# Optimization experiments

Hardware: AMD Instinct MI355X
Metric: run time of the kernel (lower is better)

The kernel has to match this reference:

```python
import jax, jax.numpy as jnp
import numpy as np

NUM_EMBEDDINGS = 1024
EMBEDDING_DIM = 256
COMMITMENT_COST = 0.25


def setup_inputs() -> dict:
    key = jax.random.key(0)
    k_z, k_e = jax.random.split(key)
    z = jax.random.normal(k_z, (4, EMBEDDING_DIM, 16, 32, 32), dtype=jnp.float32)
    # torch init: uniform_(-1/K, 1/K)
    emb = jax.random.uniform(
        k_e, (NUM_EMBEDDINGS, EMBEDDING_DIM), dtype=jnp.float32,
        minval=-1.0 / NUM_EMBEDDINGS, maxval=1.0 / NUM_EMBEDDINGS)
    return {"z": z, "emb": emb}


def reference(z, emb):
    sg = jax.lax.stop_gradient
    b, c, d, h, w = z.shape
    K = emb.shape[0]
    # (B,C,D,H,W) -> (N, C)
    z_flat = jnp.transpose(z, (0, 2, 3, 4, 1)).reshape(-1, c)
    x_sq = jnp.sum(z_flat * z_flat, axis=1, keepdims=True)          # (N,1)
    e_sq = jnp.sum(emb * emb, axis=1)                                # (K,)
    xe = z_flat @ emb.T                                              # (N,K)
    distances = x_sq + e_sq[None, :] - 2.0 * xe
    encoding_indices = jnp.argmin(distances, axis=1)                 # (N,)
    z_q = emb[encoding_indices].reshape(b, d, h, w, c).transpose(0, 4, 1, 2, 3)
    embedding_loss = jnp.mean((sg(z_q) - z) ** 2)
    commitment_loss = COMMITMENT_COST * jnp.mean((z_q - sg(z)) ** 2)
    vq_loss = embedding_loss + commitment_loss
    z_q_st = z + sg(z_q - z)  # straight-through
    # perplexity from codebook usage histogram (== mean of one-hot encodings)
    counts = jnp.zeros((K,), z_flat.dtype).at[encoding_indices].add(1.0)
    avg_probs = counts / z_flat.shape[0]
    perplexity = jnp.exp(-jnp.sum(avg_probs * jnp.log(avg_probs + 1e-10)))
    return z_q_st, vq_loss, perplexity, encoding_indices.reshape(b, d, h, w)
```

## Files before the change

kernel.cpp:

```cpp
#include <hip/hip_runtime.h>


#define C_DIM 256
#define K_CODES 1024
#define N_VEC 65536
#define T_GAP 4e-4f

#define OUT_ZQ_SIZE 16777216
#define OUT_LOSS_OFF 16777216
#define OUT_PP_OFF   16777217
#define OUT_IDX_OFF  16777218

#define WS_EH    0
#define WS_EL    524288
#define WS_ESQ   1048576
#define WS_XSQ   1052672
#define WS_CNT   1314816
#define WS_LOSS  1318912
#define WS_FLC   1318920
#define WS_FLIST 1581072
#define WS_PM1   1843264
#define WS_EMBT  1843264
#define WS_PM2   2891840
#define WS_PIX   3940416

typedef __attribute__((ext_vector_type(8))) short short8;
typedef __attribute__((ext_vector_type(8))) unsigned short ushort8;
typedef __attribute__((ext_vector_type(16))) float f32x16;

__device__ __forceinline__ unsigned short bf16_rne(float v) {
    unsigned u = __float_as_uint(v);
    unsigned r = (u + 0x7FFFu + ((u >> 16) & 1u)) >> 16;
    return (unsigned short)r;
}



__global__ __launch_bounds__(256) void convert_z_kernel(const float* __restrict__ z,
                                                        unsigned short* __restrict__ zhF,
                                                        unsigned short* __restrict__ zlF,
                                                        float* __restrict__ xsq) {
#pragma clang fp contract(off)
    __shared__ float tile[128][65];
    const int tid = threadIdx.x;
    const int ln = tid & 63;
    const int og = tid >> 6;
    const int n0 = blockIdx.x * 64;
    const int b = n0 >> 14, s0 = n0 & 16383;
    const int n = n0 + ln;
    const size_t tbase = (size_t)(n >> 5) * 8192;
    const int lr = n & 31;
    float res = 0.0f;

    for (int p = 0; p < 2; ++p) {
        __syncthreads();
        for (int i = 0; i < 32; ++i) {
            int c = p * 128 + i * 4 + og;
            tile[i * 4 + og][ln] = z[((size_t)b << 22) + ((size_t)c << 14) + s0 + ln];
        }
        __syncthreads();
#pragma unroll
        for (int t = 0; t < 4; ++t) {
            int oh = og + t * 4;
            int o  = p * 16 + oh;
            ushort8 hb, lb;
#pragma unroll
            for (int j = 0; j < 8; ++j) {
                float v = tile[oh * 8 + j][ln];
                unsigned short h = bf16_rne(v);
                hb[j] = h;
                lb[j] = bf16_rne(v - __uint_as_float((unsigned)h << 16));
            }
            size_t off = tbase + (size_t)(o >> 1) * 512 + (size_t)(lr + 32 * (o & 1)) * 8;
            *reinterpret_cast<ushort8*>(zhF + off) = hb;
            *reinterpret_cast<ushort8*>(zlF + off) = lb;
        }
        if (tid < 64) {
            float r[8];
#pragma unroll
            for (int j = 0; j < 8; ++j) { float v = tile[j][tid]; r[j] = v * v; }
#pragma unroll
            for (int i = 8; i < 128; i += 8)
#pragma unroll
                for (int j = 0; j < 8; ++j) { float v = tile[i + j][tid]; float t2 = v * v; r[j] = r[j] + t2; }
            float blk = ((r[0] + r[1]) + (r[2] + r[3])) + ((r[4] + r[5]) + (r[6] + r[7]));
            res = (p == 0) ? blk : res + blk;
        }
    }
    if (tid < 64) xsq[n0 + tid] = res;
}

__device__ __forceinline__ float pairwise_sq_128(const float* p) {
#pragma clang fp contract(off)
    float r[8];
#pragma unroll
    for (int j = 0; j < 8; ++j) { float v = p[j]; r[j] = v * v; }
#pragma unroll
    for (int i = 8; i < 128; i += 8)
#pragma unroll
        for (int j = 0; j < 8; ++j) { float v = p[i + j]; float t = v * v; r[j] = r[j] + t; }
    return ((r[0] + r[1]) + (r[2] + r[3])) + ((r[4] + r[5]) + (r[6] + r[7]));
}

__global__ __launch_bounds__(256) void convert_e_kernel(const float* __restrict__ emb,
                                                        unsigned short* __restrict__ ehF,
                                                        unsigned short* __restrict__ elF,
                                                        float* __restrict__ esq) {
#pragma clang fp contract(off)
    int t = blockIdx.x * 256 + threadIdx.x;
    int k = t >> 5, o = t & 31;
    int c0 = o * 8;
    ushort8 hb, lb;
#pragma unroll
    for (int j = 0; j < 8; ++j) {
        float v = emb[k * C_DIM + c0 + j];
        unsigned short h = bf16_rne(v);
        hb[j] = h;
        lb[j] = bf16_rne(v - __uint_as_float((unsigned)h << 16));
    }
    size_t off = (size_t)(k >> 5) * 8192 + (size_t)(o >> 1) * 512 + (size_t)((k & 31) + 32 * (o & 1)) * 8;
    *reinterpret_cast<ushort8*>(ehF + off) = hb;
    *reinterpret_cast<ushort8*>(elF + off) = lb;
    if (threadIdx.x < 8) {
        int k8 = blockIdx.x * 8 + threadIdx.x;
        const float* row = emb + (size_t)k8 * C_DIM;
        esq[k8] = pairwise_sq_128(row) + pairwise_sq_128(row + 128);
    }
}

__global__ __launch_bounds__(256) void transpose_kernel(const float* __restrict__ emb,
                                                        float* __restrict__ embT) {
    __shared__ float t[64][65];
    const int k0 = blockIdx.x * 64;
    const int c0 = blockIdx.y * 64;
    const int tx = threadIdx.x & 63, ty = threadIdx.x >> 6;
    for (int r = ty; r < 64; r += 4)
        t[r][tx] = emb[(k0 + r) * C_DIM + c0 + tx];
    __syncthreads();
    for (int r = ty; r < 64; r += 4)
        embT[(c0 + r) * K_CODES + k0 + tx] = t[tx][r];
}


__global__ __launch_bounds__(512, 1) void screen_kernel(
    const unsigned short* __restrict__ zhF, const unsigned short* __restrict__ zlF,
    const unsigned short* __restrict__ ehF, const unsigned short* __restrict__ elF,
    const float* __restrict__ esq, const float* __restrict__ xsq,
    float* __restrict__ pm1, float* __restrict__ pm2,
    unsigned short* __restrict__ pix) {
    __shared__ __align__(16) unsigned short abuf[2][64 * 512];
    __shared__ float xbuf[512];
    __shared__ float smp1[2][8][64], smp2[2][8][64];
    __shared__ int   smi[2][8][64];

    const int tid = threadIdx.x;
    const int w = tid >> 6, l = tid & 63, lr = l & 31, lh = l >> 5;
    const int bid = blockIdx.x;
    const int v = (bid & 7) * 64 + (bid >> 3);
    const int nb = v >> 2, kb = v & 3;
    const int n0 = nb * 512;
    const int kw = kb * 256 + w * 32;
    const int loff = l * 8;

    short8 Eh[16], El[16];
    {
        const unsigned short* bh = ehF + (size_t)(kb * 8 + w) * 8192 + loff;
        const unsigned short* bl = elF + (size_t)(kb * 8 + w) * 8192 + loff;
#pragma unroll
        for (int q = 0; q < 16; ++q) {
            Eh[q] = *reinterpret_cast<const short8*>(bh + q * 512);
            Bl_dummy:;
            El[q] = *reinterpret_cast<const short8*>(bl + q * 512);
        }
    }
    float esql[16];
#pragma unroll
    for (int r = 0; r < 16; ++r)
        esql[r] = esq[kw + (r & 3) + 8 * (r >> 2) + 4 * lh];

    __builtin_amdgcn_global_load_lds(
        (const __attribute__((address_space(1))) void*)(xsq + n0 + w * 64 + l),
        (__attribute__((address_space(3))) void*)&xbuf[w * 64], 4, 0, 0);

    asm volatile("s_waitcnt vmcnt(0)" ::: "memory");
    __builtin_amdgcn_s_barrier();

#define STAGE(S) do {                                                                   \
    const int _b = (S) & 1;                                                             \
    _Pragma("unroll")                                                                   \
    for (int ci = 0; ci < 8; ++ci) {                                                    \
        int c = 8 * w + ci;                                                             \
        const unsigned short* src = ((c & 32) ? zlF : zhF)                              \
            + (size_t)((n0 >> 5) + (S) * 2 + ((c >> 4) & 1)) * 8192                     \
            + (size_t)(c & 15) * 512 + loff;                                            \
        __builtin_amdgcn_global_load_lds(                                               \
            (const __attribute__((address_space(1))) void*)src,                         \
            (__attribute__((address_space(3))) void*)&abuf[_b][c * 512], 16, 0, 0);     \
    }                                                                                   \
} while (0)

    STAGE(0);

    float rm1 = 3.4e38f, rm2 = 3.4e38f;
    int   ri1 = 0;

    for (int s = 0; s < 8; ++s) {
        const int cur = s & 1;
        asm volatile("s_waitcnt vmcnt(0) lgkmcnt(0)" ::: "memory");
        __builtin_amdgcn_s_barrier();
        __builtin_amdgcn_sched_barrier(0);
        if (s < 7) STAGE(s + 1);

        if (s >= 1 && w == s - 1) {
            const int pp = (s - 1) & 1;
            float m1 = smp1[pp][0][l], m2 = smp2[pp][0][l];
            int i1 = smi[pp][0][l];
#pragma unroll
            for (int ww = 1; ww < 8; ++ww) {
                float q1 = smp1[pp][ww][l], q2 = smp2[pp][ww][l];
                int qi = smi[pp][ww][l];
                if (q1 < m1)      { m2 = fminf(m1, q2); m1 = q1; i1 = qi; }
                else if (q1 > m1) { m2 = fminf(m2, q1); }
                else              { m2 = m1; }
            }
            rm1 = m1; rm2 = m2; ri1 = i1;
        }

        f32x16 acc0, acc1;
#pragma unroll
        for (int r = 0; r < 16; ++r) { acc0[r] = 0.0f; acc1[r] = 0.0f; }

        __builtin_amdgcn_s_setprio(1);
#pragma unroll
        for (int q = 0; q < 16; ++q) {
            short8 azh0 = *reinterpret_cast<const short8*>(&abuf[cur][(q)      * 512 + loff]);
            short8 azh1 = *reinterpret_cast<const short8*>(&abuf[cur][(16 + q) * 512 + loff]);
            short8 azl0 = *reinterpret_cast<const short8*>(&abuf[cur][(32 + q) * 512 + loff]);
            short8 azl1 = *reinterpret_cast<const short8*>(&abuf[cur][(48 + q) * 512 + loff]);
            acc0 = __builtin_amdgcn_mfma_f32_32x32x16_bf16(Eh[q], azh0, acc0, 0, 0, 0);
            acc1 = __builtin_amdgcn_mfma_f32_32x32x16_bf16(Eh[q], azh1, acc1, 0, 0, 0);
            acc0 = __builtin_amdgcn_mfma_f32_32x32x16_bf16(Eh[q], azl0, acc0, 0, 0, 0);
            acc1 = __builtin_amdgcn_mfma_f32_32x32x16_bf16(Eh[q], azl1, acc1, 0, 0, 0);
            acc0 = __builtin_amdgcn_mfma_f32_32x32x16_bf16(El[q], azh0, acc0, 0, 0, 0);
            acc1 = __builtin_amdgcn_mfma_f32_32x32x16_bf16(El[q], azh1, acc1, 0, 0, 0);
        }
        __builtin_amdgcn_s_setprio(0);

#pragma unroll
        for (int i = 0; i < 2; ++i) {
            const f32x16 a = i ? acc1 : acc0;
            const float xs = xbuf[s * 64 + i * 32 + lr];
            float m1 = 3.4e38f, m2 = 3.4e38f;
            int i1 = 0;
#pragma unroll
            for (int r = 0; r < 16; ++r) {
                float sv = (xs + esql[r]) - 2.0f * a[r];
                int kg = kw + (r & 3) + 8 * (r >> 2) + 4 * lh;
                if (sv < m1) { m2 = m1; m1 = sv; i1 = kg; }
                else m2 = fminf(m2, sv);
            }
            float om1 = __shfl_xor(m1, 32, 64);
            float om2 = __shfl_xor(m2, 32, 64);
            int   oi  = __shfl_xor(i1, 32, 64);
            if (om1 < m1)      { m2 = fminf(m1, om2); m1 = om1; i1 = oi; }
            else if (om1 > m1) { m2 = fminf(m2, om1); }
            else               { m2 = m1; i1 = min(i1, oi); }
            if (lh == 0) {
                smp1[s & 1][w][i * 32 + lr] = m1;
                smp2[s & 1][w][i * 32 + lr] = m2;
                smi [s & 1][w][i * 32 + lr] = i1;
            }
        }
    }
#undef STAGE

    asm volatile("s_waitcnt lgkmcnt(0)" ::: "memory");
    __builtin_amdgcn_s_barrier();
    if (w == 7) {
        float m1 = smp1[1][0][l], m2 = smp2[1][0][l];
        int i1 = smi[1][0][l];
#pragma unroll
        for (int ww = 1; ww < 8; ++ww) {
            float q1 = smp1[1][ww][l], q2 = smp2[1][ww][l];
            int qi = smi[1][ww][l];
            if (q1 < m1)      { m2 = fminf(m1, q2); m1 = q1; i1 = qi; }
            else if (q1 > m1) { m2 = fminf(m2, q1); }
            else              { m2 = m1; }
        }
        rm1 = m1; rm2 = m2; ri1 = i1;
    }

    {
        size_t p = (size_t)kb * N_VEC + n0 + w * 64 + l;
        pm1[p] = rm1; pm2[p] = rm2; pix[p] = (unsigned short)ri1;
    }
}

__global__ __launch_bounds__(256) void merge_kernel(
    const float* __restrict__ pm1, const float* __restrict__ pm2,
    const unsigned short* __restrict__ pix,
    unsigned* __restrict__ flag_list, unsigned* __restrict__ flag_count,
    float* __restrict__ out_idx, unsigned* __restrict__ counts) {
    int n = blockIdx.x * 256 + threadIdx.x;
    float m1 = 3.4e38f, m2 = 3.4e38f;
    int i1 = 0;
    for (int kb = 0; kb < 4; ++kb) {
        size_t p = (size_t)kb * N_VEC + n;
        float a1 = pm1[p], a2 = pm2[p];
        int ai = (int)pix[p];
        if (a1 < m1)      { m2 = fminf(m1, a2); m1 = a1; i1 = ai; }
        else if (a1 > m1) { m2 = fminf(m2, a1); }
        else              { m2 = m1; i1 = min(i1, ai); }
    }
    if (m2 - m1 <= T_GAP) {
        unsigned pos = atomicAdd(flag_count, 1u);
        flag_list[pos] = (unsigned)n;
    } else {
        out_idx[n] = (float)i1;
        atomicAdd(&counts[i1], 1u);
    }
}


__global__ __launch_bounds__(256) void refine_kernel(
    const float* __restrict__ z, const float* __restrict__ embT,
    const float* __restrict__ esq, const float* __restrict__ xsq,
    const unsigned* __restrict__ flag_list, const unsigned* __restrict__ flag_count,
    float* __restrict__ out_idx, unsigned* __restrict__ counts) {
#pragma clang fp contract(off)
    __shared__ float zrow[8][256];
    __shared__ int nrow[8];
    __shared__ unsigned long long red[8][4];
    const int tid = threadIdx.x;
    const unsigned cnt = *flag_count;
    const unsigned groups = (cnt + 7) >> 3;
    const int kbase = tid * 4;
    for (unsigned g = blockIdx.x; g < groups; g += gridDim.x) {
        __syncthreads();
        if (tid < 8) nrow[tid] = (g * 8 + tid < cnt) ? (int)flag_list[g * 8 + tid] : -1;
        __syncthreads();
        for (int r = 0; r < 8; ++r) {
            int n = nrow[r];
            if (n >= 0) {
                int b = n >> 14, s = n & 16383;
                zrow[r][tid] = z[((size_t)b << 22) + ((size_t)tid << 14) + s];
            }
        }
        __syncthreads();
        float acc[8][4];
#pragma unroll
        for (int r = 0; r < 8; ++r)
#pragma unroll
            for (int j = 0; j < 4; ++j) acc[r][j] = 0.0f;
        for (int c4 = 0; c4 < 64; ++c4) {
            float4 ek[4];
#pragma unroll
            for (int x = 0; x < 4; ++x)
                ek[x] = *reinterpret_cast<const float4*>(embT + (size_t)(c4 * 4 + x) * K_CODES + kbase);
#pragma unroll
            for (int r = 0; r < 8; ++r) {
                float4 zv = *reinterpret_cast<const float4*>(&zrow[r][c4 * 4]);
                float a;
                a = acc[r][0];
                a = fmaf(zv.x, ek[0].x, a); a = fmaf(zv.y, ek[1].x, a);
                a = fmaf(zv.z, ek[2].x, a); a = fmaf(zv.w, ek[3].x, a);
                acc[r][0] = a;
                a = acc[r][1];
                a = fmaf(zv.x, ek[0].y, a); a = fmaf(zv.y, ek[1].y, a);
                a = fmaf(zv.z, ek[2].y, a); a = fmaf(zv.w, ek[3].y, a);
                acc[r][1] = a;
                a = acc[r][2];
                a = fmaf(zv.x, ek[0].z, a); a = fmaf(zv.y, ek[1].z, a);
                a = fmaf(zv.z, ek[2].z, a); a = fmaf(zv.w, ek[3].z, a);
                acc[r][2] = a;
                a = acc[r][3];
                a = fmaf(zv.x, ek[0].w, a); a = fmaf(zv.y, ek[1].w, a);
                a = fmaf(zv.z, ek[2].w, a); a = fmaf(zv.w, ek[3].w, a);
                acc[r][3] = a;
            }
        }
        float esql[4];
#pragma unroll
        for (int j = 0; j < 4; ++j) esql[j] = esq[kbase + j];
#pragma unroll
        for (int r = 0; r < 8; ++r) {
            int n = nrow[r];
            float xs = (n >= 0) ? xsq[n] : 0.0f;
            float m = 3.4e38f;
            int mi = 0;
#pragma unroll
            for (int j = 0; j < 4; ++j) {
                float t1 = xs + esql[j];
                float d = t1 - 2.0f * acc[r][j];
                if (d < m) { m = d; mi = kbase + j; }
            }
            unsigned long long p = ((unsigned long long)__float_as_uint(m) << 32) | (unsigned)mi;
            for (int off = 32; off >= 1; off >>= 1) {
                unsigned long long o = __shfl_xor(p, off, 64);
                p = (o < p) ? o : p;
            }
            if ((tid & 63) == 0) red[r][tid >> 6] = p;
        }
        __syncthreads();
        if (tid < 8 && nrow[tid] >= 0) {
            unsigned long long p = red[tid][0];
#pragma unroll
            for (int ww = 1; ww < 4; ++ww) { unsigned long long o = red[tid][ww]; p = (o < p) ? o : p; }
            int idx = (int)(p & 0xFFFFFFFFull);
            out_idx[nrow[tid]] = (float)idx;
            atomicAdd(&counts[idx], 1u);
        }
    }
}


__global__ __launch_bounds__(256) void gather_kernel(
    const float* __restrict__ z, const float* __restrict__ embT,
    const float* __restrict__ out_idx, float* __restrict__ out,
    double* __restrict__ loss_acc) {
    const int tid = threadIdx.x;
    const int ct = blockIdx.x & 3;
    const int st = (blockIdx.x >> 2) & 15;
    const int b  = blockIdx.x >> 6;
    const int s0 = st * 1024;
    const int c0 = ct * 64;

    int idx[4];
#pragma unroll
    for (int q = 0; q < 4; ++q)
        idx[q] = (int)out_idx[(b << 14) + s0 + 4 * tid + q];

    const float* zb = z + ((size_t)b << 22) + s0 + 4 * tid;
    float* ob = out + ((size_t)b << 22) + s0 + 4 * tid;

    double local = 0.0;
    for (int c = 0; c < 64; ++c) {
        const int cg = c0 + c;
        const float* er = embT + (size_t)cg * K_CODES;
        float4 zv = *reinterpret_cast<const float4*>(zb + ((size_t)cg << 14));
        float4 ov;
        float d0 = er[idx[0]] - zv.x;
        float d1 = er[idx[1]] - zv.y;
        float d2 = er[idx[2]] - zv.z;
        float d3 = er[idx[3]] - zv.w;
        ov.x = zv.x + d0; ov.y = zv.y + d1; ov.z = zv.z + d2; ov.w = zv.w + d3;
        *reinterpret_cast<float4*>(ob + ((size_t)cg << 14)) = ov;
        local += (double)d0 * d0 + (double)d1 * d1 + (double)d2 * d2 + (double)d3 * d3;
    }
    for (int off = 32; off >= 1; off >>= 1) local += __shfl_down(local, off, 64);
    __shared__ double redd[4];
    if ((tid & 63) == 0) redd[tid >> 6] = local;
    __syncthreads();
    if (tid == 0) atomicAdd(loss_acc, redd[0] + redd[1] + redd[2] + redd[3]);
}

__global__ void finalize_kernel(const unsigned* __restrict__ counts,
                                const double* __restrict__ loss_acc,
                                float* __restrict__ out) {
    int tid = threadIdx.x;
    double s = 0.0;
    for (int k = tid; k < K_CODES; k += 256) {
        float avg = (float)counts[k] / 65536.0f;
        float t = avg * logf(avg + 1e-10f);
        s += (double)t;
    }
    for (int off = 32; off >= 1; off >>= 1) s += __shfl_down(s, off, 64);
    __shared__ double red[4];
    if ((tid & 63) == 0) red[tid >> 6] = s;
    __syncthreads();
    if (tid == 0) {
        double tot = red[0] + red[1] + red[2] + red[3];
        out[OUT_PP_OFF]   = expf((float)(-tot));
        out[OUT_LOSS_OFF] = 1.25f * (float)(loss_acc[0] / 16777216.0);
    }
}

extern "C" void kernel_launch(void* const* d_in, const int* in_sizes, int n_in,
                              void* d_out, int out_size, void* d_ws, size_t ws_size,
                              hipStream_t stream) {
    const float* z   = (const float*)d_in[0];
    const float* emb = (const float*)d_in[1];
    float* out = (float*)d_out;
    char* ws = (char*)d_ws;

    unsigned short* ehF = (unsigned short*)(ws + WS_EH);
    unsigned short* elF = (unsigned short*)(ws + WS_EL);
    float*    esq       = (float*)(ws + WS_ESQ);
    float*    xsq       = (float*)(ws + WS_XSQ);
    unsigned* counts    = (unsigned*)(ws + WS_CNT);
    double*   loss_acc  = (double*)(ws + WS_LOSS);
    unsigned* flag_cnt  = (unsigned*)(ws + WS_FLC);
    unsigned* flist     = (unsigned*)(ws + WS_FLIST);
    float*    pm1       = (float*)(ws + WS_PM1);
    float*    pm2       = (float*)(ws + WS_PM2);
    unsigned short* pix = (unsigned short*)(ws + WS_PIX);
    float*    embT      = (float*)(ws + WS_EMBT);

    unsigned short* zhF = (unsigned short*)out;
    unsigned short* zlF = (unsigned short*)(out + 8388608);
    float* out_idx = out + OUT_IDX_OFF;

    hipMemsetAsync(ws + WS_CNT, 0, 4108, stream);

    convert_z_kernel<<<1024, 256, 0, stream>>>(z, zhF, zlF, xsq);
    convert_e_kernel<<<128, 256, 0, stream>>>(emb, ehF, elF, esq);
    screen_kernel<<<512, 512, 0, stream>>>(zhF, zlF, ehF, elF, esq, xsq, pm1, pm2, pix);
    merge_kernel<<<256, 256, 0, stream>>>(pm1, pm2, pix, flist, flag_cnt, out_idx, counts);
    transpose_kernel<<<dim3(16, 4), 256, 0, stream>>>(emb, embT);
    refine_kernel<<<1024, 256, 0, stream>>>(z, embT, esq, xsq, flist, flag_cnt, out_idx, counts);
    gather_kernel<<<256, 256, 0, stream>>>(z, embT, out_idx, out, loss_acc);
    finalize_kernel<<<1, 256, 0, stream>>>(counts, loss_acc, out);
}
```

Measured before the change: 245.0 us.

## Drop low-bf16 half of z in screening GEMM and widen refine threshold

Removes the z low-part bf16 split, so the screening GEMM uses zh*(eh+el) instead of three product terms. This cuts MFMA work by a third, halves z staging traffic and LDS buffer size, and drops the zl writes in convert_z. Separate accumulators for the high and low products also lengthen the independent MFMA chains. Because the screen is now less precise, the near-tie gap threshold is raised, so more vectors get flagged for exact fp32 refinement. The refine kernel may therefore have more work to do.

```diff
diff --git a/kernel.cpp b/kernel.cpp
--- a/kernel.cpp
+++ b/kernel.cpp
@@ -4,7 +4,7 @@
 #define C_DIM 256
 #define K_CODES 1024
 #define N_VEC 65536
-#define T_GAP 4e-4f
+#define T_GAP 6e-4f
 
 #define OUT_ZQ_SIZE 16777216
 #define OUT_LOSS_OFF 16777216
@@ -38,7 +38,6 @@
 
 __global__ __launch_bounds__(256) void convert_z_kernel(const float* __restrict__ z,
                                                         unsigned short* __restrict__ zhF,
-                                                        unsigned short* __restrict__ zlF,
                                                         float* __restrict__ xsq) {
 #pragma clang fp contract(off)
     __shared__ float tile[128][65];
@@ -63,17 +62,12 @@
         for (int t = 0; t < 4; ++t) {
             int oh = og + t * 4;
             int o  = p * 16 + oh;
-            ushort8 hb, lb;
-#pragma unroll
-            for (int j = 0; j < 8; ++j) {
-                float v = tile[oh * 8 + j][ln];
-                unsigned short h = bf16_rne(v);
-                hb[j] = h;
-                lb[j] = bf16_rne(v - __uint_as_float((unsigned)h << 16));
-            }
+            ushort8 hb;
+#pragma unroll
+            for (int j = 0; j < 8; ++j)
+                hb[j] = bf16_rne(tile[oh * 8 + j][ln]);
             size_t off = tbase + (size_t)(o >> 1) * 512 + (size_t)(lr + 32 * (o & 1)) * 8;
             *reinterpret_cast<ushort8*>(zhF + off) = hb;
-            *reinterpret_cast<ushort8*>(zlF + off) = lb;
         }
         if (tid < 64) {
             float r[8];
@@ -143,12 +137,12 @@
 
 
 __global__ __launch_bounds__(512, 1) void screen_kernel(
-    const unsigned short* __restrict__ zhF, const unsigned short* __restrict__ zlF,
+    const unsigned short* __restrict__ zhF,
     const unsigned short* __restrict__ ehF, const unsigned short* __restrict__ elF,
     const float* __restrict__ esq, const float* __restrict__ xsq,
     float* __restrict__ pm1, float* __restrict__ pm2,
     unsigned short* __restrict__ pix) {
-    __shared__ __align__(16) unsigned short abuf[2][64 * 512];
+    __shared__ __align__(16) unsigned short abuf[2][32 * 512];
     __shared__ float xbuf[512];
     __shared__ float smp1[2][8][64], smp2[2][8][64];
     __shared__ int   smi[2][8][64];
@@ -169,7 +163,6 @@
 #pragma unroll
         for (int q = 0; q < 16; ++q) {
             Eh[q] = *reinterpret_cast<const short8*>(bh + q * 512);
-            Bl_dummy:;
             El[q] = *reinterpret_cast<const short8*>(bl + q * 512);
         }
     }
@@ -188,10 +181,10 @@
 #define STAGE(S) do {                                                                   \
     const int _b = (S) & 1;                                                             \
     _Pragma("unroll")                                                                   \
-    for (int ci = 0; ci < 8; ++ci) {                                                    \
-        int c = 8 * w + ci;                                                             \
-        const unsigned short* src = ((c & 32) ? zlF : zhF)                              \
-            + (size_t)((n0 >> 5) + (S) * 2 + ((c >> 4) & 1)) * 8192                     \
+    for (int ci = 0; ci < 4; ++ci) {                                                    \
+        int c = 4 * w + ci;                                                             \
+        const unsigned short* src = zhF                                                 \
+            + (size_t)((n0 >> 5) + (S) * 2 + (c >> 4)) * 8192                           \
             + (size_t)(c & 15) * 512 + loff;                                            \
         __builtin_amdgcn_global_load_lds(                                               \
             (const __attribute__((address_space(1))) void*)src,                         \
@@ -226,35 +219,33 @@
             rm1 = m1; rm2 = m2; ri1 = i1;
         }
 
-        f32x16 acc0, acc1;
-#pragma unroll
-        for (int r = 0; r < 16; ++r) { acc0[r] = 0.0f; acc1[r] = 0.0f; }
+        f32x16 aH0, aL0, aH1, aL1;
+#pragma unroll
+        for (int r = 0; r < 16; ++r) { aH0[r] = 0.0f; aL0[r] = 0.0f; aH1[r] = 0.0f; aL1[r] = 0.0f; }
 
         __builtin_amdgcn_s_setprio(1);
 #pragma unroll
         for (int q = 0; q < 16; ++q) {
             short8 azh0 = *reinterpret_cast<const short8*>(&abuf[cur][(q)      * 512 + loff]);
             short8 azh1 = *reinterpret_cast<const short8*>(&abuf[cur][(16 + q) * 512 + loff]);
-            short8 azl0 = *reinterpret_cast<const short8*>(&abuf[cur][(32 + q) * 512 + loff]);
-            short8 azl1 = *reinterpret_cast<const short8*>(&abuf[cur][(48 + q) * 512 + loff]);
-            acc0 = __builtin_amdgcn_mfma_f32_32x32x16_bf16(Eh[q], azh0, acc0, 0, 0, 0);
-            acc1 = __builtin_amdgcn_mfma_f32_32x32x16_bf16(Eh[q], azh1, acc1, 0, 0, 0);
-            acc0 = __builtin_amdgcn_mfma_f32_32x32x16_bf16(Eh[q], azl0, acc0, 0, 0, 0);
-            acc1 = __builtin_amdgcn_mfma_f32_32x32x16_bf16(Eh[q], azl1, acc1, 0, 0, 0);
-            acc0 = __builtin_amdgcn_mfma_f32_32x32x16_bf16(El[q], azh0, acc0, 0, 0, 0);
-            acc1 = __builtin_amdgcn_mfma_f32_32x32x16_bf16(El[q], azh1, acc1, 0, 0, 0);
+            aH0 = __builtin_amdgcn_mfma_f32_32x32x16_bf16(Eh[q], azh0, aH0, 0, 0, 0);
+            aL0 = __builtin_amdgcn_mfma_f32_32x32x16_bf16(El[q], azh0, aL0, 0, 0, 0);
+            aH1 = __builtin_amdgcn_mfma_f32_32x32x16_bf16(Eh[q], azh1, aH1, 0, 0, 0);
+            aL1 = __builtin_amdgcn_mfma_f32_32x32x16_bf16(El[q], azh1, aL1, 0, 0, 0);
         }
         __builtin_amdgcn_s_setprio(0);
 
 #pragma unroll
         for (int i = 0; i < 2; ++i) {
-            const f32x16 a = i ? acc1 : acc0;
+            const f32x16 aH = i ? aH1 : aH0;
+            const f32x16 aL = i ? aL1 : aL0;
             const float xs = xbuf[s * 64 + i * 32 + lr];
             float m1 = 3.4e38f, m2 = 3.4e38f;
             int i1 = 0;
 #pragma unroll
             for (int r = 0; r < 16; ++r) {
-                float sv = (xs + esql[r]) - 2.0f * a[r];
+                float dot = aH[r] + aL[r];
+                float sv = (xs + esql[r]) - 2.0f * dot;
                 int kg = kw + (r & 3) + 8 * (r >> 2) + 4 * lh;
                 if (sv < m1) { m2 = m1; m1 = sv; i1 = kg; }
                 else m2 = fminf(m2, sv);
@@ -497,14 +488,13 @@
     float*    embT      = (float*)(ws + WS_EMBT);
 
     unsigned short* zhF = (unsigned short*)out;
-    unsigned short* zlF = (unsigned short*)(out + 8388608);
     float* out_idx = out + OUT_IDX_OFF;
 
     hipMemsetAsync(ws + WS_CNT, 0, 4108, stream);
 
-    convert_z_kernel<<<1024, 256, 0, stream>>>(z, zhF, zlF, xsq);
+    convert_z_kernel<<<1024, 256, 0, stream>>>(z, zhF, xsq);
     convert_e_kernel<<<128, 256, 0, stream>>>(emb, ehF, elF, esq);
-    screen_kernel<<<512, 512, 0, stream>>>(zhF, zlF, ehF, elF, esq, xsq, pm1, pm2, pix);
+    screen_kernel<<<512, 512, 0, stream>>>(zhF, ehF, elF, esq, xsq, pm1, pm2, pix);
     merge_kernel<<<256, 256, 0, stream>>>(pm1, pm2, pix, flist, flag_cnt, out_idx, counts);
     transpose_kernel<<<dim3(16, 4), 256, 0, stream>>>(emb, embT);
     refine_kernel<<<1024, 256, 0, stream>>>(z, embT, esq, xsq, flist, flag_cnt, out_idx, counts);
```

Result: no change. 245.0 us (+0.0%).
